# Kernel optimization log

Measured on AMD Instinct MI355X. Metric: run time of the kernel, lower is better.

## Reference

```python
import jax, jax.numpy as jnp
import numpy as np

B, C, D = 16384, 16, 768
H = D // 2  # bottleneck dim of Specializer


def setup_inputs() -> dict:
    key = jax.random.key(0)
    k1, k2, k3, k4 = jax.random.split(key, 4)
    return {
        "embedding": jax.random.normal(k1, (B, D), dtype=jnp.float32),
        "logits": jax.random.normal(k2, (B, C), dtype=jnp.float32),
        "w1": jax.random.normal(k3, (C, D, H), dtype=jnp.float32) * 0.02,
        "b1": jnp.zeros((C, H), dtype=jnp.float32),
        "w4": jax.random.normal(k4, (C, H, D), dtype=jnp.float32) * 0.02,
        "b4": jnp.zeros((C, D), dtype=jnp.float32),
    }


def _l2norm(x, eps):
    # F.normalize(x, dim=-1, eps=eps): x / max(||x||_2, eps)
    n = jnp.sqrt(jnp.sum(x * x, axis=-1, keepdims=True))
    return x / jnp.maximum(n, eps)


def reference(embedding, logits, w1, b1, w4, b4):
    # cls(): softmax(logits/10), top-1 mask, gated weights
    gate = jax.nn.softmax(logits / 10.0, axis=-1)           # [B, C]
    top1 = jnp.argmax(gate, axis=-1)                        # [B]
    gate = gate * jax.nn.one_hot(top1, C, dtype=gate.dtype)  # scatter mask * gate

    # embedder(): run ALL experts densely (as the torch code does)
    h = jax.nn.relu(jnp.einsum('bd,cdh->bch', embedding, w1) + b1)  # [B, C, H]
    e = jnp.einsum('bch,chd->bcd', h, w4) + b4                      # [B, C, D]
    comb = jnp.einsum('bcd,bc->bd', e, gate)                        # [B, D]
    comb = _l2norm(comb, 1e-6)
    out = comb + embedding
    # normalize=True -> F.normalize with default eps 1e-12
    return _l2norm(out, 1e-12)
```

## Files before the change

kernel.cpp:

```cpp
#include <hip/hip_runtime.h>
#include <stdint.h>


#define B_ROWS 16384
#define C_EXP  16
#define D_DIM  768
#define H_DIM  384

typedef __bf16 bf16_t;
typedef __bf16 bf16x8 __attribute__((ext_vector_type(8)));
typedef float  f32x4  __attribute__((ext_vector_type(4)));

static constexpr size_t WS_CNT  = 0;
static constexpr size_t WS_CUR  = 64;
static constexpr size_t WS_OFF  = 128;
static constexpr size_t WS_TOFF = 256;
static constexpr size_t WS_EXP  = 512;
static constexpr size_t WS_GATE = WS_EXP  + (size_t)B_ROWS * 4;
static constexpr size_t WS_ROW  = WS_GATE + (size_t)B_ROWS * 4;
static constexpr size_t WS_W1   = WS_ROW  + (size_t)B_ROWS * 4;
static constexpr size_t W_BYTES = (size_t)C_EXP * D_DIM * H_DIM * 2;
static constexpr size_t WS_W4   = WS_W1 + W_BYTES;
static constexpr size_t WS_END  = WS_W4 + W_BYTES;


__device__ __forceinline__ f32x4 mfma16(bf16x8 a, bf16x8 b, f32x4 c) {
    return __builtin_amdgcn_mfma_f32_16x16x32_bf16(a, b, c, 0, 0, 0);
}

__global__ __launch_bounds__(512) void prep(const float* __restrict__ w1,
                                            const float* __restrict__ w4,
                                            const float* __restrict__ logits,
                                            char* __restrict__ w1s,
                                            char* __restrict__ w4s,
                                            int* __restrict__ expert,
                                            float* __restrict__ gatev,
                                            int* __restrict__ cnt) {
    __shared__ float tile[64 * 65];
    __shared__ int   hist[16];
    int bid = blockIdx.x;

    if (bid >= 2304) {
        if (threadIdx.x < 16) hist[threadIdx.x] = 0;
        __syncthreads();
        int b = (bid - 2304) * 512 + threadIdx.x;
        const f32x4* lp = (const f32x4*)(logits + (size_t)b * C_EXP);
        float l[16];
#pragma unroll
        for (int i = 0; i < 4; ++i) {
            f32x4 v = lp[i];
            l[i*4+0] = v[0]; l[i*4+1] = v[1]; l[i*4+2] = v[2]; l[i*4+3] = v[3];
        }
        float m = l[0]; int idx = 0;
#pragma unroll
        for (int j = 1; j < 16; ++j)
            if (l[j] > m) { m = l[j]; idx = j; }
        float s = 0.f;
#pragma unroll
        for (int j = 0; j < 16; ++j) s += __expf((l[j] - m) * 0.1f);
        expert[b] = idx;
        gatev[b]  = 1.0f / s;
        atomicAdd(&hist[idx], 1);
        __syncthreads();
        if (threadIdx.x < 16) {
            int c = hist[threadIdx.x];
            if (c) atomicAdd(&cnt[threadIdx.x], c);
        }
        return;
    }

    bool is1 = bid < 1152;
    int lb = is1 ? bid : bid - 1152;
    int c = lb / 72, rem = lb % 72;
    int kc, nb, Nfull, KF, NF;
    const float* src;
    char* dstbase;
    if (is1) {
        kc = rem / 6;  nb = rem % 6;  Nfull = H_DIM; KF = 24; NF = 24;
        src     = w1 + (size_t)c * D_DIM * H_DIM;
        dstbase = w1s;
    } else {
        kc = rem / 12; nb = rem % 12; Nfull = D_DIM; KF = 12; NF = 48;
        src     = w4 + (size_t)c * H_DIM * D_DIM;
        dstbase = w4s;
    }
#pragma unroll
    for (int it = 0; it < 2; ++it) {
        int f  = threadIdx.x + it * 512;
        int kr = f >> 4, nq = f & 15;
        f32x4 v = *(const f32x4*)(src + (size_t)(kc * 64 + kr) * Nfull + nb * 64 + nq * 4);
        tile[kr * 65 + nq * 4 + 0] = v[0];
        tile[kr * 65 + nq * 4 + 1] = v[1];
        tile[kr * 65 + nq * 4 + 2] = v[2];
        tile[kr * 65 + nq * 4 + 3] = v[3];
    }
    __syncthreads();
    {
        int frag = threadIdx.x >> 6, lane = threadIdx.x & 63;
        int kfl  = frag >> 2, nfl = frag & 3;
        int col  = lane & 15, kq = lane >> 4;
        bf16x8 p;
#pragma unroll
        for (int j = 0; j < 8; ++j)
            p[j] = (bf16_t)tile[(kfl * 32 + kq * 8 + j) * 65 + nfl * 16 + col];
        int kf = kc * 2 + kfl, nf = nb * 4 + nfl;
        size_t off = (((size_t)c * KF + kf) * NF + nf) * 1024 + lane * 16;
        *(bf16x8*)(dstbase + off) = p;
    }
}

__global__ void scank(const int* __restrict__ cnt, int* __restrict__ offs,
                      int* __restrict__ toff) {
    if (threadIdx.x == 0 && blockIdx.x == 0) {
        int o = 0, to = 0;
        for (int e = 0; e < C_EXP; ++e) {
            offs[e] = o; toff[e] = to;
            o  += cnt[e];
            to += (cnt[e] + 31) >> 5;
        }
        offs[C_EXP] = o; toff[C_EXP] = to;
    }
}

__global__ __launch_bounds__(512) void scatk(const int* __restrict__ expert,
                                             const int* __restrict__ offs,
                                             int* __restrict__ cursor,
                                             int* __restrict__ rowlist) {
    __shared__ int lcur[16], lbase[16];
    int b = blockIdx.x * 512 + threadIdx.x;
    if (threadIdx.x < 16) lcur[threadIdx.x] = 0;
    __syncthreads();
    int e = expert[b];
    int p = atomicAdd(&lcur[e], 1);
    __syncthreads();
    if (threadIdx.x < 16) {
        int c = lcur[threadIdx.x];
        lbase[threadIdx.x] = c ? atomicAdd(&cursor[threadIdx.x], c) : 0;
    }
    __syncthreads();
    rowlist[offs[e] + lbase[e] + p] = b;
}

#define SMEM_BYTES 76032

__global__ __launch_bounds__(512, 4) void moe_main(
    const float* __restrict__ emb, const float* __restrict__ gatev,
    const int* __restrict__ rowlist, const int* __restrict__ cnt,
    const int* __restrict__ offs, const int* __restrict__ toff,
    const char* __restrict__ w1s, const char* __restrict__ w4s,
    const float* __restrict__ b1, const float* __restrict__ b4,
    float* __restrict__ out) {
    extern __shared__ char smem[];

    int bid = blockIdx.x;
    int t   = (bid & 7) * 66 + (bid >> 3);

    int total = toff[C_EXP];
    if (t >= total) return;
    int e = 0;
#pragma unroll
    for (int i = 1; i < C_EXP; ++i) e = (t >= toff[i]) ? i : e;
    int tin  = t - toff[e];
    int Meff = cnt[e] - tin * 32; if (Meff > 32) Meff = 32;
    int base = offs[e] + tin * 32;

    int*   ridxL = (int*)(smem + 75776);
    float* gateL = (float*)(smem + 75904);
    float* ssb1  = (float*)(smem + 73728);
    float* ssb2  = (float*)(smem + 74752);
    if (threadIdx.x < 32) {
        int rr = threadIdx.x;
        int p  = base + (rr < Meff ? rr : 0);
        int ri = rowlist[p];
        ridxL[rr] = ri;
        gateL[rr] = gatev[ri];
    }

    const int wid  = threadIdx.x >> 6;
    const int lane = threadIdx.x & 63;
    const int l15  = lane & 15, l4 = lane >> 4;

    const char* w1e = w1s + (size_t)e * 589824;
    const char* w4e = w4s + (size_t)e * 589824;

    auto ldB1 = [&](int kf, int jn) {
        return *(const bf16x8*)(w1e + ((size_t)(kf * 24 + wid * 3 + jn)) * 1024 + lane * 16);
    };
    auto ldB4 = [&](int kf, int jn) {
        return *(const bf16x8*)(w4e + ((size_t)(kf * 48 + wid * 6 + jn)) * 1024 + lane * 16);
    };
    bf16x8 cb0 = ldB1(0, 0), cb1 = ldB1(0, 1), cb2 = ldB1(0, 2);

    __syncthreads();

#pragma unroll
    for (int it = 0; it < 6; ++it) {
        int q   = threadIdx.x + it * 512;
        int row = q / 96, kq = q % 96;
        const float* s = emb + (size_t)ridxL[row] * D_DIM + kq * 8;
        f32x4 f0 = *(const f32x4*)s;
        f32x4 f1 = *(const f32x4*)(s + 4);
        bf16x8 p;
        p[0]=(bf16_t)f0[0]; p[1]=(bf16_t)f0[1]; p[2]=(bf16_t)f0[2]; p[3]=(bf16_t)f0[3];
        p[4]=(bf16_t)f1[0]; p[5]=(bf16_t)f1[1]; p[6]=(bf16_t)f1[2]; p[7]=(bf16_t)f1[3];
        *(bf16x8*)(smem + row * 1536 + ((kq * 16) ^ ((row & 7) << 4))) = p;
    }
    __syncthreads();

    f32x4 acc1[2][3];
#pragma unroll
    for (int rg = 0; rg < 2; ++rg)
#pragma unroll
        for (int j = 0; j < 3; ++j) acc1[rg][j] = f32x4{0.f, 0.f, 0.f, 0.f};

#pragma unroll
    for (int kf = 0; kf < 24; ++kf) {
        bf16x8 nb0, nb1, nb2;
        if (kf + 1 < 24) { nb0 = ldB1(kf+1, 0); nb1 = ldB1(kf+1, 1); nb2 = ldB1(kf+1, 2); }
        int kb = (kf * 32 + l4 * 8) * 2;
        bf16x8 a0 = *(const bf16x8*)(smem + l15 * 1536 + (kb ^ ((l15 & 7) << 4)));
        bf16x8 a1 = *(const bf16x8*)(smem + (l15 + 16) * 1536 + (kb ^ ((l15 & 7) << 4)));
        acc1[0][0] = mfma16(a0, cb0, acc1[0][0]);
        acc1[1][0] = mfma16(a1, cb0, acc1[1][0]);
        acc1[0][1] = mfma16(a0, cb1, acc1[0][1]);
        acc1[1][1] = mfma16(a1, cb1, acc1[1][1]);
        acc1[0][2] = mfma16(a0, cb2, acc1[0][2]);
        acc1[1][2] = mfma16(a1, cb2, acc1[1][2]);
        if (kf + 1 < 24) { cb0 = nb0; cb1 = nb1; cb2 = nb2; }
    }

    bf16x8 db0 = ldB4(0, 0), db1 = ldB4(0, 1), db2 = ldB4(0, 2);
    bf16x8 db3 = ldB4(0, 3), db4 = ldB4(0, 4), db5 = ldB4(0, 5);

#pragma unroll
    for (int jn = 0; jn < 3; ++jn) {
        int col = wid * 48 + jn * 16 + l15;
        float bb = b1[e * H_DIM + col];
#pragma unroll
        for (int rg = 0; rg < 2; ++rg)
#pragma unroll
            for (int v = 0; v < 4; ++v) {
                int row = rg * 16 + l4 * 4 + v;
                float hv = fmaxf(acc1[rg][jn][v] + bb, 0.f);
                *(bf16_t*)(smem + 49152 + row * 768 + ((col * 2) ^ ((row & 7) << 4))) = (bf16_t)hv;
            }
    }
    __syncthreads();

    f32x4 acc2[2][6];
#pragma unroll
    for (int rg = 0; rg < 2; ++rg)
#pragma unroll
        for (int j = 0; j < 6; ++j) acc2[rg][j] = f32x4{0.f, 0.f, 0.f, 0.f};

#pragma unroll
    for (int kf = 0; kf < 12; ++kf) {
        bf16x8 nb0, nb1, nb2, nb3, nb4, nb5;
        if (kf + 1 < 12) {
            nb0 = ldB4(kf+1, 0); nb1 = ldB4(kf+1, 1); nb2 = ldB4(kf+1, 2);
            nb3 = ldB4(kf+1, 3); nb4 = ldB4(kf+1, 4); nb5 = ldB4(kf+1, 5);
        }
        int kb = (kf * 32 + l4 * 8) * 2;
        bf16x8 a0 = *(const bf16x8*)(smem + 49152 + l15 * 768 + (kb ^ ((l15 & 7) << 4)));
        bf16x8 a1 = *(const bf16x8*)(smem + 49152 + (l15 + 16) * 768 + (kb ^ ((l15 & 7) << 4)));
        acc2[0][0] = mfma16(a0, db0, acc2[0][0]);
        acc2[1][0] = mfma16(a1, db0, acc2[1][0]);
        acc2[0][1] = mfma16(a0, db1, acc2[0][1]);
        acc2[1][1] = mfma16(a1, db1, acc2[1][1]);
        acc2[0][2] = mfma16(a0, db2, acc2[0][2]);
        acc2[1][2] = mfma16(a1, db2, acc2[1][2]);
        acc2[0][3] = mfma16(a0, db3, acc2[0][3]);
        acc2[1][3] = mfma16(a1, db3, acc2[1][3]);
        acc2[0][4] = mfma16(a0, db4, acc2[0][4]);
        acc2[1][4] = mfma16(a1, db4, acc2[1][4]);
        acc2[0][5] = mfma16(a0, db5, acc2[0][5]);
        acc2[1][5] = mfma16(a1, db5, acc2[1][5]);
        if (kf + 1 < 12) { db0 = nb0; db1 = nb1; db2 = nb2; db3 = nb3; db4 = nb4; db5 = nb5; }
    }

    const int colb = wid * 96;
    float part[2][4];
#pragma unroll
    for (int rg = 0; rg < 2; ++rg)
#pragma unroll
        for (int v = 0; v < 4; ++v) part[rg][v] = 0.f;

#pragma unroll
    for (int jn = 0; jn < 6; ++jn) {
        float bb = b4[e * D_DIM + colb + jn * 16 + l15];
#pragma unroll
        for (int rg = 0; rg < 2; ++rg)
#pragma unroll
            for (int v = 0; v < 4; ++v) {
                float cv = (acc2[rg][jn][v] + bb) * gateL[rg * 16 + l4 * 4 + v];
                acc2[rg][jn][v] = cv;
                part[rg][v] += cv * cv;
            }
    }
#pragma unroll
    for (int o = 1; o < 16; o <<= 1)
#pragma unroll
        for (int rg = 0; rg < 2; ++rg)
#pragma unroll
            for (int v = 0; v < 4; ++v) part[rg][v] += __shfl_xor(part[rg][v], o, 64);
    if (l15 == 0)
#pragma unroll
        for (int rg = 0; rg < 2; ++rg)
#pragma unroll
            for (int v = 0; v < 4; ++v) ssb1[(rg * 16 + l4 * 4 + v) * 8 + wid] = part[rg][v];
    __syncthreads();

    int   rloc[2][4];
    size_t rbase[2][4];
    float inv1[2][4];
#pragma unroll
    for (int rg = 0; rg < 2; ++rg)
#pragma unroll
        for (int v = 0; v < 4; ++v) {
            int row = rg * 16 + l4 * 4 + v;
            rloc[rg][v]  = row;
            rbase[rg][v] = (size_t)ridxL[row] * D_DIM;
            float s = 0.f;
#pragma unroll
            for (int w = 0; w < 8; ++w) s += ssb1[row * 8 + w];
            inv1[rg][v] = 1.0f / fmaxf(sqrtf(s), 1e-6f);
        }

    float part2[2][4];
#pragma unroll
    for (int rg = 0; rg < 2; ++rg)
#pragma unroll
        for (int v = 0; v < 4; ++v) part2[rg][v] = 0.f;

#pragma unroll
    for (int jn = 0; jn < 6; ++jn) {
        int col = colb + jn * 16 + l15;
#pragma unroll
        for (int rg = 0; rg < 2; ++rg)
#pragma unroll
            for (int v = 0; v < 4; ++v) {
                float em = emb[rbase[rg][v] + col];
                float o2 = acc2[rg][jn][v] * inv1[rg][v] + em;
                acc2[rg][jn][v] = o2;
                part2[rg][v] += o2 * o2;
            }
    }
#pragma unroll
    for (int o = 1; o < 16; o <<= 1)
#pragma unroll
        for (int rg = 0; rg < 2; ++rg)
#pragma unroll
            for (int v = 0; v < 4; ++v) part2[rg][v] += __shfl_xor(part2[rg][v], o, 64);
    if (l15 == 0)
#pragma unroll
        for (int rg = 0; rg < 2; ++rg)
#pragma unroll
            for (int v = 0; v < 4; ++v) ssb2[rloc[rg][v] * 8 + wid] = part2[rg][v];
    __syncthreads();

#pragma unroll
    for (int rg = 0; rg < 2; ++rg)
#pragma unroll
        for (int v = 0; v < 4; ++v) {
            float s = 0.f;
#pragma unroll
            for (int w = 0; w < 8; ++w) s += ssb2[rloc[rg][v] * 8 + w];
            float inv2 = 1.0f / fmaxf(sqrtf(s), 1e-12f);
            if (rloc[rg][v] < Meff) {
#pragma unroll
                for (int jn = 0; jn < 6; ++jn)
                    out[rbase[rg][v] + colb + jn * 16 + l15] = acc2[rg][jn][v] * inv2;
            }
        }
}

extern "C" void kernel_launch(void* const* d_in, const int* in_sizes, int n_in,
                              void* d_out, int out_size, void* d_ws, size_t ws_size,
                              hipStream_t stream) {
    const float* emb    = (const float*)d_in[0];
    const float* logits = (const float*)d_in[1];
    const float* w1     = (const float*)d_in[2];
    const float* b1     = (const float*)d_in[3];
    const float* w4     = (const float*)d_in[4];
    const float* b4     = (const float*)d_in[5];
    float* out = (float*)d_out;
    char*  ws  = (char*)d_ws;
    if (ws_size < WS_END) return;

    int*   cnt     = (int*)(ws + WS_CNT);
    int*   cur     = (int*)(ws + WS_CUR);
    int*   offs    = (int*)(ws + WS_OFF);
    int*   toff    = (int*)(ws + WS_TOFF);
    int*   expert  = (int*)(ws + WS_EXP);
    float* gatev   = (float*)(ws + WS_GATE);
    int*   rowlist = (int*)(ws + WS_ROW);
    char*  w1s     = ws + WS_W1;
    char*  w4s     = ws + WS_W4;

    hipMemsetAsync(ws, 0, 512, stream);
    prep<<<dim3(2336), dim3(512), 0, stream>>>(w1, w4, logits, w1s, w4s,
                                               expert, gatev, cnt);
    scank<<<dim3(1), dim3(64), 0, stream>>>(cnt, offs, toff);
    scatk<<<dim3(32), dim3(512), 0, stream>>>(expert, offs, cur, rowlist);

    (void)hipFuncSetAttribute((const void*)moe_main,
                              hipFuncAttributeMaxDynamicSharedMemorySize, SMEM_BYTES);
    moe_main<<<dim3(528), dim3(512), SMEM_BYTES, stream>>>(
        emb, gatev, rowlist, cnt, offs, toff, w1s, w4s, b1, b4, out);
}
```

Measured before the change: 94.42 us.

## Alias hidden-activation buffer onto input tile and raise occupancy to six blocks

The hidden activation tile now reuses the LDS region of the bf16 input tile, with an added barrier between the two uses, so shared memory per block drops from about 76 KB to about 51 KB. Launch bounds go from 4 to 6 blocks per CU. Explicit register double-buffering of weight fragments is removed and weights are loaded inline per MFMA, which frees registers and relies on the extra waves to hide load latency. Row bases become 32-bit offsets to save registers. The risk is exposed global-load latency if the compiler does not schedule loads early, plus one extra barrier per block.

```diff
diff --git a/kernel.cpp b/kernel.cpp
--- a/kernel.cpp
+++ b/kernel.cpp
@@ -141,9 +141,9 @@
     rowlist[offs[e] + lbase[e] + p] = b;
 }
 
-#define SMEM_BYTES 76032
-
-__global__ __launch_bounds__(512, 4) void moe_main(
+#define SMEM_BYTES 51456
+
+__global__ __launch_bounds__(512, 6) void moe_main(
     const float* __restrict__ emb, const float* __restrict__ gatev,
     const int* __restrict__ rowlist, const int* __restrict__ cnt,
     const int* __restrict__ offs, const int* __restrict__ toff,
@@ -164,10 +164,10 @@
     int Meff = cnt[e] - tin * 32; if (Meff > 32) Meff = 32;
     int base = offs[e] + tin * 32;
 
-    int*   ridxL = (int*)(smem + 75776);
-    float* gateL = (float*)(smem + 75904);
-    float* ssb1  = (float*)(smem + 73728);
-    float* ssb2  = (float*)(smem + 74752);
+    float* ssb1  = (float*)(smem + 49152);
+    float* ssb2  = (float*)(smem + 50176);
+    int*   ridxL = (int*)(smem + 51200);
+    float* gateL = (float*)(smem + 51328);
     if (threadIdx.x < 32) {
         int rr = threadIdx.x;
         int p  = base + (rr < Meff ? rr : 0);
@@ -175,6 +175,7 @@
         ridxL[rr] = ri;
         gateL[rr] = gatev[ri];
     }
+    __syncthreads();
 
     const int wid  = threadIdx.x >> 6;
     const int lane = threadIdx.x & 63;
@@ -182,16 +183,6 @@
 
     const char* w1e = w1s + (size_t)e * 589824;
     const char* w4e = w4s + (size_t)e * 589824;
-
-    auto ldB1 = [&](int kf, int jn) {
-        return *(const bf16x8*)(w1e + ((size_t)(kf * 24 + wid * 3 + jn)) * 1024 + lane * 16);
-    };
-    auto ldB4 = [&](int kf, int jn) {
-        return *(const bf16x8*)(w4e + ((size_t)(kf * 48 + wid * 6 + jn)) * 1024 + lane * 16);
-    };
-    bf16x8 cb0 = ldB1(0, 0), cb1 = ldB1(0, 1), cb2 = ldB1(0, 2);
-
-    __syncthreads();
 
 #pragma unroll
     for (int it = 0; it < 6; ++it) {
@@ -215,22 +206,17 @@
 
 #pragma unroll
     for (int kf = 0; kf < 24; ++kf) {
-        bf16x8 nb0, nb1, nb2;
-        if (kf + 1 < 24) { nb0 = ldB1(kf+1, 0); nb1 = ldB1(kf+1, 1); nb2 = ldB1(kf+1, 2); }
         int kb = (kf * 32 + l4 * 8) * 2;
         bf16x8 a0 = *(const bf16x8*)(smem + l15 * 1536 + (kb ^ ((l15 & 7) << 4)));
         bf16x8 a1 = *(const bf16x8*)(smem + (l15 + 16) * 1536 + (kb ^ ((l15 & 7) << 4)));
-        acc1[0][0] = mfma16(a0, cb0, acc1[0][0]);
-        acc1[1][0] = mfma16(a1, cb0, acc1[1][0]);
-        acc1[0][1] = mfma16(a0, cb1, acc1[0][1]);
-        acc1[1][1] = mfma16(a1, cb1, acc1[1][1]);
-        acc1[0][2] = mfma16(a0, cb2, acc1[0][2]);
-        acc1[1][2] = mfma16(a1, cb2, acc1[1][2]);
-        if (kf + 1 < 24) { cb0 = nb0; cb1 = nb1; cb2 = nb2; }
-    }
-
-    bf16x8 db0 = ldB4(0, 0), db1 = ldB4(0, 1), db2 = ldB4(0, 2);
-    bf16x8 db3 = ldB4(0, 3), db4 = ldB4(0, 4), db5 = ldB4(0, 5);
+#pragma unroll
+        for (int jn = 0; jn < 3; ++jn) {
+            bf16x8 b = *(const bf16x8*)(w1e + ((size_t)(kf * 24 + wid * 3 + jn)) * 1024 + lane * 16);
+            acc1[0][jn] = mfma16(a0, b, acc1[0][jn]);
+            acc1[1][jn] = mfma16(a1, b, acc1[1][jn]);
+        }
+    }
+    __syncthreads();
 
 #pragma unroll
     for (int jn = 0; jn < 3; ++jn) {
@@ -242,7 +228,7 @@
             for (int v = 0; v < 4; ++v) {
                 int row = rg * 16 + l4 * 4 + v;
                 float hv = fmaxf(acc1[rg][jn][v] + bb, 0.f);
-                *(bf16_t*)(smem + 49152 + row * 768 + ((col * 2) ^ ((row & 7) << 4))) = (bf16_t)hv;
+                *(bf16_t*)(smem + row * 768 + ((col * 2) ^ ((row & 7) << 4))) = (bf16_t)hv;
             }
     }
     __syncthreads();
@@ -255,27 +241,15 @@
 
 #pragma unroll
     for (int kf = 0; kf < 12; ++kf) {
-        bf16x8 nb0, nb1, nb2, nb3, nb4, nb5;
-        if (kf + 1 < 12) {
-            nb0 = ldB4(kf+1, 0); nb1 = ldB4(kf+1, 1); nb2 = ldB4(kf+1, 2);
-            nb3 = ldB4(kf+1, 3); nb4 = ldB4(kf+1, 4); nb5 = ldB4(kf+1, 5);
-        }
         int kb = (kf * 32 + l4 * 8) * 2;
-        bf16x8 a0 = *(const bf16x8*)(smem + 49152 + l15 * 768 + (kb ^ ((l15 & 7) << 4)));
-        bf16x8 a1 = *(const bf16x8*)(smem + 49152 + (l15 + 16) * 768 + (kb ^ ((l15 & 7) << 4)));
-        acc2[0][0] = mfma16(a0, db0, acc2[0][0]);
-        acc2[1][0] = mfma16(a1, db0, acc2[1][0]);
-        acc2[0][1] = mfma16(a0, db1, acc2[0][1]);
-        acc2[1][1] = mfma16(a1, db1, acc2[1][1]);
-        acc2[0][2] = mfma16(a0, db2, acc2[0][2]);
-        acc2[1][2] = mfma16(a1, db2, acc2[1][2]);
-        acc2[0][3] = mfma16(a0, db3, acc2[0][3]);
-        acc2[1][3] = mfma16(a1, db3, acc2[1][3]);
-        acc2[0][4] = mfma16(a0, db4, acc2[0][4]);
-        acc2[1][4] = mfma16(a1, db4, acc2[1][4]);
-        acc2[0][5] = mfma16(a0, db5, acc2[0][5]);
-        acc2[1][5] = mfma16(a1, db5, acc2[1][5]);
-        if (kf + 1 < 12) { db0 = nb0; db1 = nb1; db2 = nb2; db3 = nb3; db4 = nb4; db5 = nb5; }
+        bf16x8 a0 = *(const bf16x8*)(smem + l15 * 768 + (kb ^ ((l15 & 7) << 4)));
+        bf16x8 a1 = *(const bf16x8*)(smem + (l15 + 16) * 768 + (kb ^ ((l15 & 7) << 4)));
+#pragma unroll
+        for (int jn = 0; jn < 6; ++jn) {
+            bf16x8 b = *(const bf16x8*)(w4e + ((size_t)(kf * 48 + wid * 6 + jn)) * 1024 + lane * 16);
+            acc2[0][jn] = mfma16(a0, b, acc2[0][jn]);
+            acc2[1][jn] = mfma16(a1, b, acc2[1][jn]);
+        }
     }
 
     const int colb = wid * 96;
@@ -310,16 +284,14 @@
             for (int v = 0; v < 4; ++v) ssb1[(rg * 16 + l4 * 4 + v) * 8 + wid] = part[rg][v];
     __syncthreads();
 
-    int   rloc[2][4];
-    size_t rbase[2][4];
+    int   rofs[2][4];
     float inv1[2][4];
 #pragma unroll
     for (int rg = 0; rg < 2; ++rg)
 #pragma unroll
         for (int v = 0; v < 4; ++v) {
             int row = rg * 16 + l4 * 4 + v;
-            rloc[rg][v]  = row;
-            rbase[rg][v] = (size_t)ridxL[row] * D_DIM;
+            rofs[rg][v] = ridxL[row] * D_DIM;
             float s = 0.f;
 #pragma unroll
             for (int w = 0; w < 8; ++w) s += ssb1[row * 8 + w];
@@ -339,7 +311,7 @@
         for (int rg = 0; rg < 2; ++rg)
 #pragma unroll
             for (int v = 0; v < 4; ++v) {
-                float em = emb[rbase[rg][v] + col];
+                float em = emb[rofs[rg][v] + col];
                 float o2 = acc2[rg][jn][v] * inv1[rg][v] + em;
                 acc2[rg][jn][v] = o2;
                 part2[rg][v] += o2 * o2;
@@ -355,21 +327,22 @@
 #pragma unroll
         for (int rg = 0; rg < 2; ++rg)
 #pragma unroll
-            for (int v = 0; v < 4; ++v) ssb2[rloc[rg][v] * 8 + wid] = part2[rg][v];
+            for (int v = 0; v < 4; ++v) ssb2[(rg * 16 + l4 * 4 + v) * 8 + wid] = part2[rg][v];
     __syncthreads();
 
 #pragma unroll
     for (int rg = 0; rg < 2; ++rg)
 #pragma unroll
         for (int v = 0; v < 4; ++v) {
+            int row = rg * 16 + l4 * 4 + v;
             float s = 0.f;
 #pragma unroll
-            for (int w = 0; w < 8; ++w) s += ssb2[rloc[rg][v] * 8 + w];
+            for (int w = 0; w < 8; ++w) s += ssb2[row * 8 + w];
             float inv2 = 1.0f / fmaxf(sqrtf(s), 1e-12f);
-            if (rloc[rg][v] < Meff) {
+            if (row < Meff) {
 #pragma unroll
                 for (int jn = 0; jn < 6; ++jn)
-                    out[rbase[rg][v] + colb + jn * 16 + l15] = acc2[rg][jn][v] * inv2;
+                    out[rofs[rg][v] + colb + jn * 16 + l15] = acc2[rg][jn][v] * inv2;
             }
         }
 }
```

New measurement: 116.4 us. 23.3% more time.
